# Kernel optimization log

Measured on AMD Instinct MI355X. Metric: run time of the kernel, lower is better.

Reference implementation:

```python
import jax, jax.numpy as jnp
import numpy as np

N = 100000
E = 1600000
IN_C, HID_C, OUT_C = 128, 64, 32


def _add_self_loops(edge_index, n):
    loops = jnp.arange(n, dtype=edge_index.dtype)
    src = jnp.concatenate([edge_index[0], loops])
    dst = jnp.concatenate([edge_index[1], loops])
    return src, dst


def _gcn_norm(src, dst, n):
    # symmetric normalization on A + I with unit edge weights
    deg = jax.ops.segment_sum(jnp.ones_like(dst, dtype=jnp.float32), dst, num_segments=n)
    dinv = jnp.where(deg > 0, jax.lax.rsqrt(deg), 0.0)
    return dinv[src] * dinv[dst]  # [E+N]


def _gcn_conv(x, src, dst, norm, W, b, n):
    h = x @ W                              # [N, out]
    msg = h[src] * norm[:, None]           # [E+N, out]  (dominant gather)
    out = jax.ops.segment_sum(msg, dst, num_segments=n)
    return out + b


def setup_inputs() -> dict:
    key = jax.random.key(0)
    k = jax.random.split(key, 6)
    x = jax.random.normal(k[0], (N, IN_C), dtype=jnp.float32)
    edge_index = jax.random.randint(k[1], (2, E), 0, N, dtype=jnp.int32)
    # Glorot-style init for GCN weights
    W1 = jax.random.normal(k[2], (IN_C, HID_C), dtype=jnp.float32) / np.sqrt(IN_C)
    b1 = jnp.zeros((HID_C,), dtype=jnp.float32)
    W2 = jax.random.normal(k[3], (HID_C, OUT_C), dtype=jnp.float32) / np.sqrt(HID_C)
    b2 = jnp.zeros((OUT_C,), dtype=jnp.float32)
    return {"x": x, "edge_index": edge_index, "W1": W1, "b1": b1, "W2": W2, "b2": b2}


def reference(x, edge_index, W1, b1, W2, b2):
    src, dst = _add_self_loops(edge_index, N)
    norm = _gcn_norm(src, dst, N)
    h = _gcn_conv(x, src, dst, norm, W1, b1, N)
    h = jax.nn.relu(h)
    # dropout p=0.2 is identity in eval mode
    out = _gcn_conv(h, src, dst, norm, W2, b2, N)
    return out
```

## Files before the change

kernel.cpp:

```cpp
#include <hip/hip_runtime.h>
#include <hip/hip_fp16.h>

#define N_NODES 100000
#define E_EDGES 1600000
#define IN_C 128
#define HID_C 64
#define OUT_C 32
#define BNODES 64
#define NBUCK ((N_NODES + BNODES - 1) / BNODES)
#define MAXB 2048
#define NCHUNK 256
#define CHUNK_E (E_EDGES / NCHUNK)

__device__ __forceinline__ int chunk_of_block(int b) { return (b & 7) * (NCHUNK / 8) + (b >> 3); }

__global__ void zero_gcur_kernel(int* __restrict__ gcur) {
    int i = blockIdx.x * 256 + threadIdx.x;
    if (i < NBUCK) gcur[i] = 0;
}

__global__ __launch_bounds__(1024) void bucket_scatter_kernel(const int* __restrict__ src,
                                                              const int* __restrict__ dst,
                                                              int* __restrict__ gcur,
                                                              unsigned* __restrict__ pairs) {
    __shared__ int h[NBUCK];
    for (int i = threadIdx.x; i < NBUCK; i += 1024) h[i] = 0;
    __syncthreads();
    const int chunk = chunk_of_block(blockIdx.x);
    const int base = chunk * CHUNK_E;
    int dc[7];
    int nj = 0;
    for (int j = threadIdx.x; j < CHUNK_E; j += 1024) {
        int d = dst[base + j];
        dc[nj++] = d;
        atomicAdd(&h[d >> 6], 1);
    }
    __syncthreads();
    for (int i = threadIdx.x; i < NBUCK; i += 1024) {
        int c = h[i];
        if (c > 0) h[i] = atomicAdd(&gcur[i], c);
    }
    __syncthreads();
    nj = 0;
    for (int j = threadIdx.x; j < CHUNK_E; j += 1024) {
        int d = dc[nj++];
        int pos = atomicAdd(&h[d >> 6], 1);
        pairs[(unsigned)(d >> 6) * MAXB + (unsigned)pos] =
            ((unsigned)src[base + j] << 6) | (unsigned)(d & 63);
    }
}

__global__ __launch_bounds__(256) void bucket_sort_kernel(const int* __restrict__ gcur,
                                                          unsigned* __restrict__ pairs,
                                                          int* __restrict__ row_beg,
                                                          int* __restrict__ row_end,
                                                          float* __restrict__ dinv) {
    __shared__ unsigned sp[MAXB];
    __shared__ int hcnt[BNODES], scn[BNODES], cur[BNODES];
    const int b = blockIdx.x;
    const int beg = b * MAXB;
    int cnt = gcur[b];
    if (cnt > MAXB) cnt = MAXB;
    if (threadIdx.x < BNODES) hcnt[threadIdx.x] = 0;
    __syncthreads();
    for (int j = threadIdx.x; j < cnt; j += 256) {
        unsigned p = pairs[beg + j];
        sp[j] = p;
        atomicAdd(&hcnt[p & 63], 1);
    }
    __syncthreads();
    if (threadIdx.x < BNODES) scn[threadIdx.x] = hcnt[threadIdx.x];
    __syncthreads();
    for (int off = 1; off < BNODES; off <<= 1) {
        int t = 0;
        if (threadIdx.x < BNODES && threadIdx.x >= off) t = scn[threadIdx.x - off];
        __syncthreads();
        if (threadIdx.x < BNODES) scn[threadIdx.x] += t;
        __syncthreads();
    }
    if (threadIdx.x < BNODES) {
        int ex = scn[threadIdx.x] - hcnt[threadIdx.x];
        cur[threadIdx.x] = ex;
        int node = b * BNODES + threadIdx.x;
        if (node < N_NODES) {
            row_beg[node] = beg + ex;
            row_end[node] = beg + ex + hcnt[threadIdx.x];
            dinv[node] = rsqrtf((float)hcnt[threadIdx.x] + 1.0f);
        }
    }
    __syncthreads();
    for (int j = threadIdx.x; j < cnt; j += 256) {
        unsigned p = sp[j];
        int pos = atomicAdd(&cur[p & 63], 1);
        pairs[beg + pos] = p >> 6;
    }
}

__global__ __launch_bounds__(256) void gemm1_kernel(const float* __restrict__ x,
                                                    const float* __restrict__ W1,
                                                    const float* __restrict__ dinv,
                                                    __half* __restrict__ hs) {
    __shared__ float sW[IN_C * HID_C];
    for (int i = threadIdx.x; i < IN_C * HID_C; i += 256) sW[i] = W1[i];
    __syncthreads();
    const int cg = (threadIdx.x & 7) * 8;
    const int row0 = blockIdx.x * 128 + (threadIdx.x >> 3) * 4;
    float acc[4][8];
#pragma unroll
    for (int r = 0; r < 4; ++r)
#pragma unroll
        for (int c = 0; c < 8; ++c) acc[r][c] = 0.f;

    int rr[4];
#pragma unroll
    for (int r = 0; r < 4; ++r) rr[r] = min(row0 + r, N_NODES - 1);

    const float4* x4 = (const float4*)x;
#pragma unroll 2
    for (int k4 = 0; k4 < IN_C / 4; ++k4) {
        float4 xv[4];
#pragma unroll
        for (int r = 0; r < 4; ++r) xv[r] = x4[(size_t)rr[r] * (IN_C / 4) + k4];
        float xs[4][4];
#pragma unroll
        for (int r = 0; r < 4; ++r) {
            xs[r][0] = xv[r].x; xs[r][1] = xv[r].y; xs[r][2] = xv[r].z; xs[r][3] = xv[r].w;
        }
#pragma unroll
        for (int kk = 0; kk < 4; ++kk) {
            const float4* wp = (const float4*)(sW + (k4 * 4 + kk) * HID_C + cg);
            float4 w0 = wp[0], w1 = wp[1];
            float wv[8] = {w0.x, w0.y, w0.z, w0.w, w1.x, w1.y, w1.z, w1.w};
#pragma unroll
            for (int r = 0; r < 4; ++r)
#pragma unroll
                for (int c = 0; c < 8; ++c)
                    acc[r][c] = fmaf(xs[r][kk], wv[c], acc[r][c]);
        }
    }
#pragma unroll
    for (int r = 0; r < 4; ++r) {
        int row = row0 + r;
        if (row < N_NODES) {
            float dv = dinv[row];
            union { float4 f; __half2 h[4]; } u;
#pragma unroll
            for (int q = 0; q < 4; ++q)
                u.h[q] = __floats2half2_rn(acc[r][2 * q] * dv, acc[r][2 * q + 1] * dv);
            *(float4*)(hs + (size_t)row * HID_C + cg) = u.f;
        }
    }
}

__global__ __launch_bounds__(256) void agg1_kernel(const int* __restrict__ row_beg,
                                                   const int* __restrict__ row_end,
                                                   const int* __restrict__ col,
                                                   const float2* __restrict__ hsf,
                                                   const float* __restrict__ dinv,
                                                   const float* __restrict__ b1,
                                                   const float* __restrict__ W2,
                                                   __half* __restrict__ gs) {
    __shared__ float sW[HID_C * OUT_C];
    __shared__ __half2 sh2[16][HID_C / 2];
    for (int i = threadIdx.x; i < HID_C * OUT_C; i += 256) sW[i] = W2[i];

    const int nl = threadIdx.x >> 4;
    const int node = blockIdx.x * 16 + nl;
    const int lane = threadIdx.x & 15;
    const int beg = row_beg[node], end = row_end[node];
    float2 u = hsf[(size_t)node * 16 + lane];
    __half2* uh = (__half2*)&u;
    float2 t0 = __half22float2(uh[0]), t1 = __half22float2(uh[1]);
    float a0 = t0.x, a1 = t0.y, a2 = t1.x, a3 = t1.y;

    int j = beg;
    int idx0 = j + (lane & 7);
    int cv = (idx0 < end) ? col[idx0] : 0;
    while (j + 8 <= end) {
        int jn = j + 8;
        int idxn = jn + (lane & 7);
        int cvn = (idxn < end) ? col[idxn] : 0;
        int s[8];
#pragma unroll
        for (int e = 0; e < 8; ++e) s[e] = __shfl(cv, e, 8);
        float2 v[8];
#pragma unroll
        for (int e = 0; e < 8; ++e) v[e] = hsf[(size_t)s[e] * 16 + lane];
        cv = cvn;
#pragma unroll
        for (int e = 0; e < 8; ++e) {
            __half2* vh = (__half2*)&v[e];
            float2 w0 = __half22float2(vh[0]), w1 = __half22float2(vh[1]);
            a0 += w0.x; a1 += w0.y; a2 += w1.x; a3 += w1.y;
        }
        j = jn;
    }
    const int tail = end - j;
    for (int e = 0; e < tail; ++e) {
        int s = __shfl(cv, e, 8);
        float2 v = hsf[(size_t)s * 16 + lane];
        __half2* vh = (__half2*)&v;
        float2 w0 = __half22float2(vh[0]), w1 = __half22float2(vh[1]);
        a0 += w0.x; a1 += w0.y; a2 += w1.x; a3 += w1.y;
    }
    const float dv = dinv[node];
    float4 bb = ((const float4*)b1)[lane];
    __half2 p0 = __floats2half2_rn(fmaxf(dv * a0 + bb.x, 0.f), fmaxf(dv * a1 + bb.y, 0.f));
    __half2 p1 = __floats2half2_rn(fmaxf(dv * a2 + bb.z, 0.f), fmaxf(dv * a3 + bb.w, 0.f));
    sh2[nl][lane * 2] = p0;
    sh2[nl][lane * 2 + 1] = p1;
    __syncthreads();

    const int oc = lane * 2;
    float o0 = 0.f, o1 = 0.f;
#pragma unroll
    for (int k2 = 0; k2 < HID_C / 2; ++k2) {
        float2 hv = __half22float2(sh2[nl][k2]);
        const float* w0 = sW + (2 * k2) * OUT_C + oc;
        const float* w1 = sW + (2 * k2 + 1) * OUT_C + oc;
        o0 = fmaf(hv.x, w0[0], o0); o1 = fmaf(hv.x, w0[1], o1);
        o0 = fmaf(hv.y, w1[0], o0); o1 = fmaf(hv.y, w1[1], o1);
    }
    *(__half2*)(gs + (size_t)node * OUT_C + oc) = __floats2half2_rn(o0 * dv, o1 * dv);
}

__global__ void agg2_kernel(const int* __restrict__ row_beg, const int* __restrict__ row_end,
                            const int* __restrict__ col,
                            const float2* __restrict__ gsf, const float* __restrict__ dinv,
                            const float* __restrict__ b2, float* __restrict__ out) {
    const int node = blockIdx.x * 32 + (threadIdx.x >> 3);
    const int lane = threadIdx.x & 7;
    if (node >= N_NODES) return;
    const int beg = row_beg[node], end = row_end[node];
    float2 u = gsf[(size_t)node * 8 + lane];
    __half2* uh = (__half2*)&u;
    float2 t0 = __half22float2(uh[0]), t1 = __half22float2(uh[1]);
    float a0 = t0.x, a1 = t0.y, a2 = t1.x, a3 = t1.y;

    int j = beg;
    int idx0 = j + lane;
    int cv = (idx0 < end) ? col[idx0] : 0;
    while (j + 8 <= end) {
        int jn = j + 8;
        int idxn = jn + lane;
        int cvn = (idxn < end) ? col[idxn] : 0;
        int s[8];
#pragma unroll
        for (int e = 0; e < 8; ++e) s[e] = __shfl(cv, e, 8);
        float2 v[8];
#pragma unroll
        for (int e = 0; e < 8; ++e) v[e] = gsf[(size_t)s[e] * 8 + lane];
        cv = cvn;
#pragma unroll
        for (int e = 0; e < 8; ++e) {
            __half2* vh = (__half2*)&v[e];
            float2 w0 = __half22float2(vh[0]), w1 = __half22float2(vh[1]);
            a0 += w0.x; a1 += w0.y; a2 += w1.x; a3 += w1.y;
        }
        j = jn;
    }
    const int tail = end - j;
    for (int e = 0; e < tail; ++e) {
        int s = __shfl(cv, e, 8);
        float2 v = gsf[(size_t)s * 8 + lane];
        __half2* vh = (__half2*)&v;
        float2 w0 = __half22float2(vh[0]), w1 = __half22float2(vh[1]);
        a0 += w0.x; a1 += w0.y; a2 += w1.x; a3 += w1.y;
    }
    float dv = dinv[node];
    float4 bb = ((const float4*)b2)[lane];
    float4 o;
    o.x = dv * a0 + bb.x;
    o.y = dv * a1 + bb.y;
    o.z = dv * a2 + bb.z;
    o.w = dv * a3 + bb.w;
    *(float4*)(out + (size_t)node * OUT_C + lane * 4) = o;
}

extern "C" void kernel_launch(void* const* d_in, const int* in_sizes, int n_in,
                              void* d_out, int out_size, void* d_ws, size_t ws_size,
                              hipStream_t stream) {
    const float* x  = (const float*)d_in[0];
    const int*   ei = (const int*)d_in[1];
    const float* W1 = (const float*)d_in[2];
    const float* b1 = (const float*)d_in[3];
    const float* W2 = (const float*)d_in[4];
    const float* b2 = (const float*)d_in[5];
    float* out = (float*)d_out;

    const int* srcv = ei;
    const int* dstv = ei + E_EDGES;

    float* dinv  = (float*)d_ws;
    __half* hs   = (__half*)(dinv + N_NODES);
    __half* gs   = hs + (size_t)N_NODES * HID_C;
    int* row_beg = (int*)(gs + (size_t)N_NODES * OUT_C);
    int* row_end = row_beg + N_NODES;
    int* gcur    = row_end + N_NODES;
    unsigned* pairs = (unsigned*)(gcur + 1568);
    int* col = (int*)pairs;

    zero_gcur_kernel<<<(NBUCK + 255) / 256, 256, 0, stream>>>(gcur);
    bucket_scatter_kernel<<<NCHUNK, 1024, 0, stream>>>(srcv, dstv, gcur, pairs);
    bucket_sort_kernel<<<NBUCK, 256, 0, stream>>>(gcur, pairs, row_beg, row_end, dinv);

    gemm1_kernel<<<(N_NODES + 127) / 128, 256, 0, stream>>>(x, W1, dinv, hs);

    agg1_kernel<<<N_NODES / 16, 256, 0, stream>>>(row_beg, row_end, col,
                                                  (const float2*)hs, dinv, b1, W2, gs);

    agg2_kernel<<<(N_NODES + 31) / 32, 256, 0, stream>>>(row_beg, row_end, col,
                                                         (const float2*)gs, dinv, b2, out);
}
```

Before: 128.7 us.

## Stage x and W1 K-chunks through shared memory in gemm1 for coalesced loads

The first-layer GEMM now loops over four K-chunks of 32. For each chunk the block cooperatively loads a padded 128x32 tile of x and a 32x64 slice of W1 into shared memory, then computes from LDS. Before, each thread loaded strided float4s of x straight from global memory and the whole W1 was staged once. The aim is coalesced global reads of x and lower LDS use per block, which may raise occupancy. The cost is extra barriers per chunk and more LDS reads of x.

```diff
diff --git a/kernel.cpp b/kernel.cpp
--- a/kernel.cpp
+++ b/kernel.cpp
@@ -100,54 +100,69 @@
                                                     const float* __restrict__ W1,
                                                     const float* __restrict__ dinv,
                                                     __half* __restrict__ hs) {
-    __shared__ float sW[IN_C * HID_C];
-    for (int i = threadIdx.x; i < IN_C * HID_C; i += 256) sW[i] = W1[i];
-    __syncthreads();
-    const int cg = (threadIdx.x & 7) * 8;
-    const int row0 = blockIdx.x * 128 + (threadIdx.x >> 3) * 4;
+    __shared__ float xt[128 * 36];
+    __shared__ float sWc[32 * 64];
+    const int row0 = blockIdx.x * 128;
+    const int colg = (threadIdx.x & 7) * 8;
+    const int rowg = (threadIdx.x >> 3) * 4;
     float acc[4][8];
 #pragma unroll
     for (int r = 0; r < 4; ++r)
 #pragma unroll
         for (int c = 0; c < 8; ++c) acc[r][c] = 0.f;
 
-    int rr[4];
-#pragma unroll
-    for (int r = 0; r < 4; ++r) rr[r] = min(row0 + r, N_NODES - 1);
-
     const float4* x4 = (const float4*)x;
-#pragma unroll 2
-    for (int k4 = 0; k4 < IN_C / 4; ++k4) {
-        float4 xv[4];
-#pragma unroll
-        for (int r = 0; r < 4; ++r) xv[r] = x4[(size_t)rr[r] * (IN_C / 4) + k4];
-        float xs[4][4];
-#pragma unroll
-        for (int r = 0; r < 4; ++r) {
-            xs[r][0] = xv[r].x; xs[r][1] = xv[r].y; xs[r][2] = xv[r].z; xs[r][3] = xv[r].w;
-        }
-#pragma unroll
-        for (int kk = 0; kk < 4; ++kk) {
-            const float4* wp = (const float4*)(sW + (k4 * 4 + kk) * HID_C + cg);
-            float4 w0 = wp[0], w1 = wp[1];
-            float wv[8] = {w0.x, w0.y, w0.z, w0.w, w1.x, w1.y, w1.z, w1.w};
-#pragma unroll
-            for (int r = 0; r < 4; ++r)
-#pragma unroll
-                for (int c = 0; c < 8; ++c)
-                    acc[r][c] = fmaf(xs[r][kk], wv[c], acc[r][c]);
-        }
-    }
-#pragma unroll
-    for (int r = 0; r < 4; ++r) {
-        int row = row0 + r;
+    const float4* w4 = (const float4*)W1;
+
+    for (int c = 0; c < 4; ++c) {
+        __syncthreads();
+#pragma unroll
+        for (int i = 0; i < 4; ++i) {
+            int g = i * 256 + threadIdx.x;
+            int r = g >> 3, k4 = g & 7;
+            int rg = min(row0 + r, N_NODES - 1);
+            float4 v = x4[(size_t)rg * (IN_C / 4) + c * 8 + k4];
+            *(float4*)(xt + r * 36 + k4 * 4) = v;
+        }
+#pragma unroll
+        for (int i = 0; i < 2; ++i) {
+            int f = i * 256 + threadIdx.x;
+            int wr = f >> 4, wc4 = f & 15;
+            *(float4*)(sWc + wr * 64 + wc4 * 4) = w4[(size_t)(c * 32 + wr) * 16 + wc4];
+        }
+        __syncthreads();
+#pragma unroll
+        for (int k4 = 0; k4 < 8; ++k4) {
+            float4 xr[4];
+#pragma unroll
+            for (int ri = 0; ri < 4; ++ri)
+                xr[ri] = *(const float4*)(xt + (rowg + ri) * 36 + k4 * 4);
+#pragma unroll
+            for (int j = 0; j < 4; ++j) {
+                const float4* wp = (const float4*)(sWc + (k4 * 4 + j) * 64 + colg);
+                float4 w0 = wp[0], w1 = wp[1];
+                float wv[8] = {w0.x, w0.y, w0.z, w0.w, w1.x, w1.y, w1.z, w1.w};
+#pragma unroll
+                for (int ri = 0; ri < 4; ++ri) {
+                    const float* xf = (const float*)&xr[ri];
+                    float xs = xf[j];
+#pragma unroll
+                    for (int cc = 0; cc < 8; ++cc)
+                        acc[ri][cc] = fmaf(xs, wv[cc], acc[ri][cc]);
+                }
+            }
+        }
+    }
+#pragma unroll
+    for (int ri = 0; ri < 4; ++ri) {
+        int row = row0 + rowg + ri;
         if (row < N_NODES) {
             float dv = dinv[row];
             union { float4 f; __half2 h[4]; } u;
 #pragma unroll
             for (int q = 0; q < 4; ++q)
-                u.h[q] = __floats2half2_rn(acc[r][2 * q] * dv, acc[r][2 * q + 1] * dv);
-            *(float4*)(hs + (size_t)row * HID_C + cg) = u.f;
+                u.h[q] = __floats2half2_rn(acc[ri][2 * q] * dv, acc[ri][2 * q + 1] * dv);
+            *(float4*)(hs + (size_t)row * HID_C + colg) = u.f;
         }
     }
 }
```

Result: faster. 126.0 us (-2.1%).
